# Performance work log

Hardware: AMD Instinct MI355X
Metric: run time of the kernel (lower is better)

The kernel has to match this reference:

```python
import jax, jax.numpy as jnp
import numpy as np

LMBDA = 100.0
GAMMA = 0.5
EPS_EV = 1e-10


def _safe_evals(e):
    return jnp.clip(jnp.nan_to_num(e, nan=EPS_EV, posinf=1e6, neginf=EPS_EV), EPS_EV, None)


def get_mask(evals1, evals2, gamma):
    # evals1, evals2: [B, K]; returns D: [B, K, K] with D[b,i,j] from (evals2[b,i], evals1[b,j])
    e1 = _safe_evals(evals1)
    e2 = _safe_evals(evals2)
    scale = jnp.clip(jnp.maximum(e1.max(axis=1), e2.max(axis=1)), 1e-10, None)[:, None]
    e1 = e1 / scale
    e2 = e2 / scale
    g1 = e1 ** gamma  # [B,K] -> broadcast as column index j
    g2 = e2 ** gamma  # [B,K] -> broadcast as row index i
    d1 = g1 * g1 + 1.0
    d2 = g2 * g2 + 1.0
    M_re = (g2 / d2)[:, :, None] - (g1 / d1)[:, None, :]
    M_im = (1.0 / d2)[:, :, None] - (1.0 / d1)[:, None, :]
    return jnp.nan_to_num(M_re * M_re + M_im * M_im, nan=0.0, posinf=1e6, neginf=0.0)


def setup_inputs() -> dict:
    key = jax.random.key(0)
    k = jax.random.split(key, 6)
    B, N, K, C = 8, 20000, 128, 256
    return {
        "feat_x": jax.random.normal(k[0], (B, N, C), dtype=jnp.float32),
        "feat_y": jax.random.normal(k[1], (B, N, C), dtype=jnp.float32),
        "evals_x": jax.random.uniform(k[2], (B, K), dtype=jnp.float32),
        "evals_y": jax.random.uniform(k[3], (B, K), dtype=jnp.float32),
        "evecs_trans_x": jax.random.normal(k[4], (B, K, N), dtype=jnp.float32),
        "evecs_trans_y": jax.random.normal(k[5], (B, K, N), dtype=jnp.float32),
    }


def reference(feat_x, feat_y, evals_x, evals_y, evecs_trans_x, evecs_trans_y):
    # Spectral projection of features: [B,K,N] @ [B,N,C] -> [B,K,C]
    A = jnp.einsum('bkn,bnc->bkc', evecs_trans_x, feat_x)
    Bm = jnp.einsum('bkn,bnc->bkc', evecs_trans_y, feat_y)
    D = get_mask(evals_x, evals_y, GAMMA)  # [B,K,K]

    A_A_t = jnp.einsum('bic,bjc->bij', A, A)   # [B,K,K]
    B_A_t = jnp.einsum('bic,bjc->bij', Bm, A)  # [B,K,K]

    K = A.shape[1]
    eye = jnp.eye(K, dtype=A.dtype)
    # lhs[b,i] = A_A_t[b] + lmbda * diag(D[b,i]) + 1e-8 * I  -> [B,K,K,K]
    lhs = A_A_t[:, None, :, :] + LMBDA * (D[..., None] * eye) + 1e-8 * eye
    rhs = B_A_t[..., None]  # [B,K,K,1]; rhs[b,i] = B_A_t[b,i,:]
    Cxy = jnp.linalg.solve(lhs, rhs)[..., 0]  # [B,K,K]; row i of Cxy = solution for eigenvalue i
    return Cxy
```

## Files before the change

kernel.cpp:

```cpp
#include <hip/hip_runtime.h>
#include <math.h>

#define B_ 8
#define N_ 20000
#define K_ 128
#define C_ 256

static_assert(N_ % 32 == 0, "N must be multiple of 32");

constexpr float LMBDA = 100.0f;
constexpr float EPS_EV = 1e-10f;

typedef unsigned int u32x4 __attribute__((ext_vector_type(4)));
typedef short short8_t __attribute__((ext_vector_type(8)));
typedef float f32x4 __attribute__((ext_vector_type(4)));

static __device__ inline void split2(float x0, float x1, unsigned& h, unsigned& l) {
  unsigned u0 = __builtin_bit_cast(unsigned, x0);
  unsigned u1 = __builtin_bit_cast(unsigned, x1);
  h = __builtin_amdgcn_perm(u1, u0, 0x07060302u);
  float r0 = x0 - __builtin_bit_cast(float, u0 & 0xFFFF0000u);
  float r1 = x1 - __builtin_bit_cast(float, u1 & 0xFFFF0000u);
  unsigned v0 = __builtin_bit_cast(unsigned, r0);
  unsigned v1 = __builtin_bit_cast(unsigned, r1);
  v0 += 0x7FFFu + ((v0 >> 16) & 1u);
  v1 += 0x7FFFu + ((v1 >> 16) & 1u);
  l = __builtin_amdgcn_perm(v1, v0, 0x07060302u);
}

#define KFENCE()                                              \
  do {                                                        \
    asm volatile("s_waitcnt lgkmcnt(0)" ::: "memory");        \
    __builtin_amdgcn_sched_barrier(0);                        \
    __builtin_amdgcn_s_barrier();                             \
    __builtin_amdgcn_sched_barrier(0);                        \
  } while (0)

__global__ __launch_bounds__(512, 4)
void proj_mfma(const float* __restrict__ feat_x, const float* __restrict__ feat_y,
               const float* __restrict__ evx, const float* __restrict__ evy,
               float* __restrict__ part, int Sa, int chunk) {
  const int bm = blockIdx.z;
  const int b = bm >> 1, mat = bm & 1;
  const float* __restrict__ E = (mat ? evy : evx) + (size_t)b * K_ * N_;
  const float* __restrict__ F = (mat ? feat_y : feat_x) + (size_t)b * N_ * C_;
  const int c0 = blockIdx.x << 7;
  const int s = blockIdx.y;
  const int nb = s * chunk;
  const int ne = min(N_, nb + chunk);
  const int nt = (ne - nb) >> 5;

  __shared__ unsigned short Ah[2][128][40];
  __shared__ unsigned short Al[2][128][40];
  __shared__ unsigned short Bh[2][128][40];
  __shared__ unsigned short Bl[2][128][40];

  const int t = threadIdx.x;
  const int lane = t & 63, wv = t >> 6;
  const int wm = wv & 3;
  const int wcc = wv >> 2;
  const int lr = lane & 15, lg = lane >> 4;

  const int am = t >> 2, ak = (t & 3) << 3;
  const int cl = t & 127, gq = (t >> 7) << 2;
  const int sigw = ((cl >> 3) & 3) << 1;
  const int slotA = ((gq >> 2) ^ sigw) << 2;
  const int slotB = (((gq >> 2) + 4) ^ sigw) << 2;

  f32x4 acc[2][4];
#pragma unroll
  for (int i = 0; i < 2; ++i)
#pragma unroll
    for (int j = 0; j < 4; ++j) acc[i][j] = (f32x4){0.f, 0.f, 0.f, 0.f};

  struct Stage { float4 a0, a1; float b0, b1, b2, b3, b4, b5, b6, b7; };

  auto LOAD = [&](Stage& st, int n0) {
    const float* ep = E + (size_t)am * N_ + n0 + ak;
    st.a0 = *(const float4*)ep;
    st.a1 = *(const float4*)(ep + 4);
    const float* fp = F + (size_t)(n0 + gq) * C_ + c0 + cl;
    st.b0 = fp[0];
    st.b1 = fp[C_];
    st.b2 = fp[2 * C_];
    st.b3 = fp[3 * C_];
    const float* fp2 = fp + (size_t)16 * C_;
    st.b4 = fp2[0];
    st.b5 = fp2[C_];
    st.b6 = fp2[2 * C_];
    st.b7 = fp2[3 * C_];
  };

  auto WRITE = [&](Stage& st, int p) {
    unsigned h01, l01, h23, l23, h45, l45, h67, l67;
    split2(st.a0.x, st.a0.y, h01, l01);
    split2(st.a0.z, st.a0.w, h23, l23);
    split2(st.a1.x, st.a1.y, h45, l45);
    split2(st.a1.z, st.a1.w, h67, l67);
    *(u32x4*)&Ah[p][am][ak] = (u32x4){h01, h23, h45, h67};
    *(u32x4*)&Al[p][am][ak] = (u32x4){l01, l23, l45, l67};
    split2(st.b0, st.b1, h01, l01);
    split2(st.b2, st.b3, h23, l23);
    *(uint2*)&Bh[p][cl][slotA] = (uint2){h01, h23};
    *(uint2*)&Bl[p][cl][slotA] = (uint2){l01, l23};
    split2(st.b4, st.b5, h45, l45);
    split2(st.b6, st.b7, h67, l67);
    *(uint2*)&Bh[p][cl][slotB] = (uint2){h45, h67};
    *(uint2*)&Bl[p][cl][slotB] = (uint2){l45, l67};
  };

  auto COMPUTE = [&](int p) {
    const int k0 = lg << 3;
    short8_t a_h[2], a_l[2];
#pragma unroll
    for (int mt = 0; mt < 2; ++mt) {
      const int m = (wm << 5) + (mt << 4) + lr;
      a_h[mt] = *(const short8_t*)&Ah[p][m][k0];
      a_l[mt] = *(const short8_t*)&Al[p][m][k0];
    }
#pragma unroll
    for (int ct = 0; ct < 4; ++ct) {
      const int c = (wcc << 6) + (ct << 4) + lr;
      const int sig = ((c >> 3) & 3) << 1;
      const int koff = (((lg << 1) ^ sig)) << 2;
      const short8_t b_h = *(const short8_t*)&Bh[p][c][koff];
      const short8_t b_l = *(const short8_t*)&Bl[p][c][koff];
#pragma unroll
      for (int mt = 0; mt < 2; ++mt) {
        acc[mt][ct] = __builtin_amdgcn_mfma_f32_16x16x32_bf16(a_h[mt], b_h, acc[mt][ct], 0, 0, 0);
        acc[mt][ct] = __builtin_amdgcn_mfma_f32_16x16x32_bf16(a_l[mt], b_h, acc[mt][ct], 0, 0, 0);
        acc[mt][ct] = __builtin_amdgcn_mfma_f32_16x16x32_bf16(a_h[mt], b_l, acc[mt][ct], 0, 0, 0);
      }
    }
  };

  Stage sA, sB;
  LOAD(sA, nb);
  if (nt > 1) LOAD(sB, nb + 32);
  WRITE(sA, 0);
  KFENCE();

  for (int it = 0; it < nt; it += 2) {
    if (it + 1 < nt) WRITE(sB, 1);
    if (it + 2 < nt) LOAD(sA, nb + ((it + 2) << 5));
    COMPUTE(0);
    KFENCE();
    if (it + 1 < nt) {
      if (it + 2 < nt) WRITE(sA, 0);
      if (it + 3 < nt) LOAD(sB, nb + ((it + 3) << 5));
      COMPUTE(1);
      KFENCE();
    }
  }

  float* __restrict__ P = part + ((size_t)bm * Sa + s) * (K_ * C_);
#pragma unroll
  for (int mt = 0; mt < 2; ++mt)
#pragma unroll
    for (int ct = 0; ct < 4; ++ct) {
      const int ccol = c0 + (wcc << 6) + (ct << 4) + lr;
#pragma unroll
      for (int r = 0; r < 4; ++r) {
        const int mrow = (wm << 5) + (mt << 4) + (lg << 2) + r;
        P[(size_t)mrow * C_ + ccol] = acc[mt][ct][r];
      }
    }
}

__global__ void reduce_parts(const float* __restrict__ part, float* __restrict__ AB, int Sa) {
  const int idx4 = blockIdx.x * 256 + threadIdx.x;
  if (idx4 >= 16 * K_ * C_ / 4) return;
  const int per = K_ * C_ / 4;
  const int bm = idx4 / per;
  const int rem4 = idx4 - bm * per;
  float4 v = {0.f, 0.f, 0.f, 0.f};
  for (int s = 0; s < Sa; ++s) {
    const float4 p = *(const float4*)&part[((size_t)bm * Sa + s) * (K_ * C_) + rem4 * 4];
    v.x += p.x; v.y += p.y; v.z += p.z; v.w += p.w;
  }
  *(float4*)&AB[(size_t)idx4 * 4] = v;
}

__global__ __launch_bounds__(256)
void gram_kernel(const float* __restrict__ AB, float* __restrict__ Sm, float* __restrict__ Rm) {
  const int b = blockIdx.x, which = blockIdx.y, qz = blockIdx.z;
  const int iq = (qz & 1) << 6, jq = (qz >> 1) << 6;
  const float* __restrict__ L  = AB + ((size_t)(b * 2 + which)) * (K_ * C_);
  const float* __restrict__ Ar = AB + ((size_t)(b * 2)) * (K_ * C_);
  float* __restrict__ out = (which ? Rm : Sm) + (size_t)b * (K_ * K_);
  const int t = threadIdx.x;
  const int ir = iq + ((t >> 4) << 2), jc = jq + ((t & 15) << 2);
  float acc[4][4] = {};
  for (int c0 = 0; c0 < C_; c0 += 4) {
    float4 li[4], rj[4];
#pragma unroll
    for (int i = 0; i < 4; ++i) li[i] = *(const float4*)(L + (size_t)(ir + i) * C_ + c0);
#pragma unroll
    for (int j = 0; j < 4; ++j) rj[j] = *(const float4*)(Ar + (size_t)(jc + j) * C_ + c0);
#pragma unroll
    for (int i = 0; i < 4; ++i)
#pragma unroll
      for (int j = 0; j < 4; ++j)
        acc[i][j] += li[i].x * rj[j].x + li[i].y * rj[j].y +
                     li[i].z * rj[j].z + li[i].w * rj[j].w;
  }
#pragma unroll
  for (int i = 0; i < 4; ++i)
#pragma unroll
    for (int j = 0; j < 4; ++j) {
      float v = acc[i][j];
      if (!which && (ir + i) == (jc + j)) v += 1e-8f;
      out[(size_t)(ir + i) * K_ + (jc + j)] = v;
    }
}

__global__ void mask_prep(const float* __restrict__ evx, const float* __restrict__ evy,
                          float* __restrict__ PQ) {
  const int b = blockIdx.x, t = threadIdx.x;
  float e1 = evx[b * K_ + t];
  float e2 = evy[b * K_ + t];
  if (e1 != e1) e1 = EPS_EV;
  if (e2 != e2) e2 = EPS_EV;
  e1 = fminf(fmaxf(e1, EPS_EV), 1e6f);
  e2 = fminf(fmaxf(e2, EPS_EV), 1e6f);

  __shared__ float wmax[2];
  float v = fmaxf(e1, e2);
#pragma unroll
  for (int d = 1; d < 64; d <<= 1) v = fmaxf(v, __shfl_xor(v, d, 64));
  if ((t & 63) == 0) wmax[t >> 6] = v;
  __syncthreads();
  const float scale = fmaxf(fmaxf(wmax[0], wmax[1]), 1e-10f);

  const float g1 = sqrtf(e1 / scale);
  const float g2 = sqrtf(e2 / scale);
  const float d1 = fmaf(g1, g1, 1.f);
  const float d2 = fmaf(g2, g2, 1.f);
  float* P = PQ + b * 512;
  P[t]       = g1 / d1;
  P[128 + t] = 1.f / d1;
  P[256 + t] = g2 / d2;
  P[384 + t] = 1.f / d2;
}

__global__ __launch_bounds__(512)
void gj_inverse(const float* __restrict__ Sm, float* __restrict__ Sinv) {
  const int b = blockIdx.x, t = threadIdx.x;
  __shared__ float a[K_ * 132];
  __shared__ float Pi[16 * 20];
  __shared__ float Rp[16 * 132];
  __shared__ float Cp[K_ * 20];
  const float* __restrict__ Sb = Sm + (size_t)b * (K_ * K_);
#pragma unroll
  for (int l = 0; l < 8; ++l) {
    int f = t + (l << 9);
    int i = f >> 5, j = (f & 31) << 2;
    *(float4*)&a[i * 132 + j] = *(const float4*)(Sb + i * K_ + j);
  }
  __syncthreads();

  const int j = t & 127, rr = t >> 7;
  const int lane = t & 63;

  for (int p = 0; p < 8; ++p) {
    const int pb = p << 4;

    if (t < 64) {
      const int r = lane & 15, g = lane >> 4;
      float4 v4 = *(const float4*)&a[(pb + r) * 132 + pb + (g << 2)];
      float vv[4] = {v4.x, v4.y, v4.z, v4.w};
#pragma unroll
      for (int k = 0; k < 16; ++k) {
        const int srcrow = (lane & 48) | k;
        float rk[4];
        rk[0] = __shfl(vv[0], srcrow);
        rk[1] = __shfl(vv[1], srcrow);
        rk[2] = __shfl(vv[2], srcrow);
        rk[3] = __shfl(vv[3], srcrow);
        const int kg = (k >> 2) << 4;
        const float pv = __shfl(vv[k & 3], kg | k);
        const float c  = __shfl(vv[k & 3], kg | r);
        const float pr = 1.0f / pv;
        float rs[4];
#pragma unroll
        for (int e = 0; e < 4; ++e) rs[e] = rk[e] * pr;
        if (r == k) {
#pragma unroll
          for (int e = 0; e < 4; ++e) vv[e] = rs[e];
          if (g == (k >> 2)) vv[k & 3] = pr;
        } else {
#pragma unroll
          for (int e = 0; e < 4; ++e) vv[e] = fmaf(-c, rs[e], vv[e]);
          if (g == (k >> 2)) vv[k & 3] = -c * pr;
        }
      }
      Pi[r * 20 + (g << 2) + 0] = vv[0];
      Pi[r * 20 + (g << 2) + 1] = vv[1];
      Pi[r * 20 + (g << 2) + 2] = vv[2];
      Pi[r * 20 + (g << 2) + 3] = vv[3];
    }
    __syncthreads();

    {
      float Ak[16];
#pragma unroll
      for (int k = 0; k < 16; ++k) Ak[k] = a[(pb + k) * 132 + j];
      const unsigned jj = (unsigned)(j - pb);
      const int r0 = rr << 2;
#pragma unroll
      for (int q = 0; q < 4; ++q) {
        const int r = r0 + q;
        float acc = 0.f;
#pragma unroll
        for (int k = 0; k < 16; ++k) acc = fmaf(Pi[r * 20 + k], Ak[k], acc);
        Rp[r * 132 + j] = (jj < 16u) ? Pi[r * 20 + jj] : acc;
      }
      const int i = j;
      const int cb = rr << 2;
      float4 cA = *(const float4*)&a[i * 132 + pb + cb];
      *(float4*)&Cp[i * 20 + cb] = cA;
    }
    __syncthreads();

    {
      float Rk[16];
#pragma unroll
      for (int k = 0; k < 16; ++k) Rk[k] = Rp[k * 132 + j];
      const unsigned jj = (unsigned)(j - pb);
      const int i0 = rr << 5;
#pragma unroll 4
      for (int m = 0; m < 32; ++m) {
        const int i = i0 + m;
        const float4 c0 = *(const float4*)&Cp[i * 20];
        const float4 c1 = *(const float4*)&Cp[i * 20 + 4];
        const float4 c2 = *(const float4*)&Cp[i * 20 + 8];
        const float4 c3 = *(const float4*)&Cp[i * 20 + 12];
        float u0 = c0.x * Rk[0] + c0.y * Rk[1] + c0.z * Rk[2] + c0.w * Rk[3];
        float u1 = c1.x * Rk[4] + c1.y * Rk[5] + c1.z * Rk[6] + c1.w * Rk[7];
        float u2 = c2.x * Rk[8] + c2.y * Rk[9] + c2.z * Rk[10] + c2.w * Rk[11];
        float u3 = c3.x * Rk[12] + c3.y * Rk[13] + c3.z * Rk[14] + c3.w * Rk[15];
        const float upd = (u0 + u1) + (u2 + u3);
        const unsigned ii = (unsigned)(i - pb);
        float newv;
        if (ii < 16u) {
          newv = Rk[ii];
        } else {
          const float base = (jj < 16u) ? 0.f : a[i * 132 + j];
          newv = base - upd;
        }
        a[i * 132 + j] = newv;
      }
    }
    __syncthreads();
  }

  float* __restrict__ O = Sinv + (size_t)b * (K_ * K_);
#pragma unroll
  for (int l = 0; l < 8; ++l) {
    int f = t + (l << 9);
    int i = f >> 5, jq = (f & 31) << 2;
    *(float4*)(O + i * K_ + jq) = *(const float4*)&a[i * 132 + jq];
  }
}

__global__ __launch_bounds__(256)
void solve_iter(const float* __restrict__ Rm, const float* __restrict__ Sinv,
                const float* __restrict__ PQ, const float* __restrict__ Xin,
                float* __restrict__ Xout, const int first) {
  const int bb = blockIdx.x;
  const int b = bb >> 2, rb = (bb & 3) << 5;
  const int t = threadIdx.x;
  __shared__ float Tt[32][34];
  __shared__ float Sv[32][132];
  __shared__ float q1[K_], p1[K_], q2l[32], p2l[32];
  {
    const float* P = PQ + b * 512;
    if (t < K_) { q1[t] = P[t]; p1[t] = P[128 + t]; }
    if (t < 32) { q2l[t] = P[256 + rb + t]; p2l[t] = P[384 + rb + t]; }
  }
  __syncthreads();
  const float* __restrict__ Rb = Rm + (size_t)b * (K_ * K_);
  const float* __restrict__ Xb = Xin + (size_t)b * (K_ * K_);
  const float* __restrict__ Si = Sinv + (size_t)b * (K_ * K_);
  const int ir = (t >> 4) << 1, jc = (t & 15) << 3;
  float acc[2][8] = {};

  for (int k0 = 0; k0 < K_; k0 += 32) {
    {
      const int i = t >> 3;
      const int kk = (t & 7) << 2;
      const int k = k0 + kk;
      const int gi = rb + i;
      float4 tv = *(const float4*)(Rb + (size_t)gi * K_ + k);
      if (!first) {
        const float4 x4 = *(const float4*)(Xb + (size_t)gi * K_ + k);
        const float qi = q2l[i], pi = p2l[i];
        float dq, dp, w;
        dq = qi - q1[k + 0]; dp = pi - p1[k + 0]; w = fmaf(dq, dq, dp * dp);
        tv.x = fmaf(-LMBDA * w, x4.x, tv.x);
        dq = qi - q1[k + 1]; dp = pi - p1[k + 1]; w = fmaf(dq, dq, dp * dp);
        tv.y = fmaf(-LMBDA * w, x4.y, tv.y);
        dq = qi - q1[k + 2]; dp = pi - p1[k + 2]; w = fmaf(dq, dq, dp * dp);
        tv.z = fmaf(-LMBDA * w, x4.z, tv.z);
        dq = qi - q1[k + 3]; dp = pi - p1[k + 3]; w = fmaf(dq, dq, dp * dp);
        tv.w = fmaf(-LMBDA * w, x4.w, tv.w);
      }
      Tt[kk + 0][i] = tv.x; Tt[kk + 1][i] = tv.y;
      Tt[kk + 2][i] = tv.z; Tt[kk + 3][i] = tv.w;
    }
#pragma unroll
    for (int l = 0; l < 4; ++l) {
      int f = t + (l << 8);
      int kk = f >> 5, j4 = (f & 31) << 2;
      *(float4*)&Sv[kk][j4] = *(const float4*)(Si + (size_t)(k0 + kk) * K_ + j4);
    }
    __syncthreads();
#pragma unroll
    for (int kk = 0; kk < 32; ++kk) {
      const float2 a2 = *(const float2*)&Tt[kk][ir];
      const float4 b0 = *(const float4*)&Sv[kk][jc];
      const float4 b1 = *(const float4*)&Sv[kk][jc + 4];
      const float bv[8] = {b0.x, b0.y, b0.z, b0.w, b1.x, b1.y, b1.z, b1.w};
#pragma unroll
      for (int jx = 0; jx < 8; ++jx) {
        acc[0][jx] = fmaf(a2.x, bv[jx], acc[0][jx]);
        acc[1][jx] = fmaf(a2.y, bv[jx], acc[1][jx]);
      }
    }
    __syncthreads();
  }

  float* __restrict__ O = Xout + (size_t)b * (K_ * K_);
#pragma unroll
  for (int i = 0; i < 2; ++i) {
    float4 o0 = {acc[i][0], acc[i][1], acc[i][2], acc[i][3]};
    float4 o1 = {acc[i][4], acc[i][5], acc[i][6], acc[i][7]};
    *(float4*)(O + (size_t)(rb + ir + i) * K_ + jc) = o0;
    *(float4*)(O + (size_t)(rb + ir + i) * K_ + jc + 4) = o1;
  }
}

extern "C" void kernel_launch(void* const* d_in, const int* in_sizes, int n_in,
                              void* d_out, int out_size, void* d_ws, size_t ws_size,
                              hipStream_t stream) {
  (void)in_sizes; (void)n_in; (void)out_size;
  const float* feat_x  = (const float*)d_in[0];
  const float* feat_y  = (const float*)d_in[1];
  const float* evals_x = (const float*)d_in[2];
  const float* evals_y = (const float*)d_in[3];
  const float* evtx    = (const float*)d_in[4];
  const float* evty    = (const float*)d_in[5];
  float* out = (float*)d_out;
  float* ws  = (float*)d_ws;

  const size_t KC16 = (size_t)16 * K_ * C_;
  const size_t KK   = (size_t)K_ * K_;
  const size_t fixed = KC16 + 3 * (KK * B_) + 4096 + 2 * (KK * B_);
  const int T = N_ / 32;

  int S = 16, Sa = 16, chunk = 0;
  for (;;) {
    int steps = (T + S - 1) / S;
    chunk = steps * 32;
    Sa = (T + steps - 1) / steps;
    if (((size_t)Sa * KC16 + fixed) * sizeof(float) <= ws_size || S == 1) break;
    S >>= 1;
  }

  float* part = ws;
  float* AB   = part + (size_t)Sa * KC16;
  float* Sm   = AB + KC16;
  float* Rm   = Sm + KK * B_;
  float* Sinv = Rm + KK * B_;
  float* PQ   = Sinv + KK * B_;
  float* X0   = PQ + 4096;
  float* X1   = X0 + KK * B_;

  mask_prep<<<dim3(8), 128, 0, stream>>>(evals_x, evals_y, PQ);
  proj_mfma<<<dim3(2, Sa, 16), 512, 0, stream>>>(feat_x, feat_y, evtx, evty, part, Sa, chunk);
  reduce_parts<<<dim3(16 * K_ * C_ / 4 / 256), 256, 0, stream>>>(part, AB, Sa);
  gram_kernel<<<dim3(8, 2, 4), 256, 0, stream>>>(AB, Sm, Rm);
  gj_inverse<<<dim3(8), 512, 0, stream>>>(Sm, Sinv);
  solve_iter<<<dim3(32), 256, 0, stream>>>(Rm, Sinv, PQ, X0, X0, 1);
  solve_iter<<<dim3(32), 256, 0, stream>>>(Rm, Sinv, PQ, X0, X1, 0);
  solve_iter<<<dim3(32), 256, 0, stream>>>(Rm, Sinv, PQ, X1, out, 0);
}
```

Baseline: 254.2 us.

## Relayout projection LDS tiles, fuse mask prep into 1024-thread inverse, reorder grid

The projection kernel now writes LDS in MFMA-fragment order in a single flat buffer, so each lane reads its operand with one contiguous vector load and no swizzle arithmetic. Each thread now loads 8 consecutive N rows for both operands. The launch grid is reordered so split-K chunks vary fastest. The mask preparation kernel is merged into the Gauss-Jordan inverse kernel, which now runs 1024 threads per block, removing one launch and spreading the elimination across more threads. The trade-offs are more LDS per inverse block, a possibly different bank-conflict pattern, and a simplified split-count choice.

```diff
diff --git a/kernel.cpp b/kernel.cpp
--- a/kernel.cpp
+++ b/kernel.cpp
@@ -44,16 +44,13 @@
   const int b = bm >> 1, mat = bm & 1;
   const float* __restrict__ E = (mat ? evy : evx) + (size_t)b * K_ * N_;
   const float* __restrict__ F = (mat ? feat_y : feat_x) + (size_t)b * N_ * C_;
-  const int c0 = blockIdx.x << 7;
-  const int s = blockIdx.y;
+  const int c0 = blockIdx.y << 7;
+  const int s = blockIdx.x;
   const int nb = s * chunk;
   const int ne = min(N_, nb + chunk);
   const int nt = (ne - nb) >> 5;
 
-  __shared__ unsigned short Ah[2][128][40];
-  __shared__ unsigned short Al[2][128][40];
-  __shared__ unsigned short Bh[2][128][40];
-  __shared__ unsigned short Bl[2][128][40];
+  __shared__ unsigned int LDSU[16384];
 
   const int t = threadIdx.x;
   const int lane = t & 63, wv = t >> 6;
@@ -61,11 +58,13 @@
   const int wcc = wv >> 2;
   const int lr = lane & 15, lg = lane >> 4;
 
-  const int am = t >> 2, ak = (t & 3) << 3;
-  const int cl = t & 127, gq = (t >> 7) << 2;
-  const int sigw = ((cl >> 3) & 3) << 1;
-  const int slotA = ((gq >> 2) ^ sigw) << 2;
-  const int slotB = (((gq >> 2) + 4) ^ sigw) << 2;
+  const int rA = ((t >> 7) << 5) | (((t >> 6) & 1) << 4) | (t & 15);
+  const int oA = (t >> 4) & 3;
+  const int cB = ((t >> 6) << 4) | (t & 15);
+  const int oB = (t >> 4) & 3;
+
+  const float* __restrict__ eb = E + (size_t)rA * N_ + (oA << 3);
+  const float* __restrict__ fb = F + (size_t)(oB << 3) * C_ + c0 + cB;
 
   f32x4 acc[2][4];
 #pragma unroll
@@ -76,55 +75,52 @@
   struct Stage { float4 a0, a1; float b0, b1, b2, b3, b4, b5, b6, b7; };
 
   auto LOAD = [&](Stage& st, int n0) {
-    const float* ep = E + (size_t)am * N_ + n0 + ak;
+    const float* ep = eb + n0;
     st.a0 = *(const float4*)ep;
     st.a1 = *(const float4*)(ep + 4);
-    const float* fp = F + (size_t)(n0 + gq) * C_ + c0 + cl;
+    const float* fp = fb + (size_t)n0 * C_;
     st.b0 = fp[0];
     st.b1 = fp[C_];
     st.b2 = fp[2 * C_];
     st.b3 = fp[3 * C_];
-    const float* fp2 = fp + (size_t)16 * C_;
-    st.b4 = fp2[0];
-    st.b5 = fp2[C_];
-    st.b6 = fp2[2 * C_];
-    st.b7 = fp2[3 * C_];
+    st.b4 = fp[4 * C_];
+    st.b5 = fp[5 * C_];
+    st.b6 = fp[6 * C_];
+    st.b7 = fp[7 * C_];
   };
 
   auto WRITE = [&](Stage& st, int p) {
-    unsigned h01, l01, h23, l23, h45, l45, h67, l67;
-    split2(st.a0.x, st.a0.y, h01, l01);
-    split2(st.a0.z, st.a0.w, h23, l23);
-    split2(st.a1.x, st.a1.y, h45, l45);
-    split2(st.a1.z, st.a1.w, h67, l67);
-    *(u32x4*)&Ah[p][am][ak] = (u32x4){h01, h23, h45, h67};
-    *(u32x4*)&Al[p][am][ak] = (u32x4){l01, l23, l45, l67};
-    split2(st.b0, st.b1, h01, l01);
-    split2(st.b2, st.b3, h23, l23);
-    *(uint2*)&Bh[p][cl][slotA] = (uint2){h01, h23};
-    *(uint2*)&Bl[p][cl][slotA] = (uint2){l01, l23};
-    split2(st.b4, st.b5, h45, l45);
-    split2(st.b6, st.b7, h67, l67);
-    *(uint2*)&Bh[p][cl][slotB] = (uint2){h45, h67};
-    *(uint2*)&Bl[p][cl][slotB] = (uint2){l45, l67};
+    const int base = (p << 13) + (t << 2);
+    unsigned h0, l0, h1, l1, h2, l2, h3, l3;
+    split2(st.a0.x, st.a0.y, h0, l0);
+    split2(st.a0.z, st.a0.w, h1, l1);
+    split2(st.a1.x, st.a1.y, h2, l2);
+    split2(st.a1.z, st.a1.w, h3, l3);
+    *(u32x4*)&LDSU[base]        = (u32x4){h0, h1, h2, h3};
+    *(u32x4*)&LDSU[base + 2048] = (u32x4){l0, l1, l2, l3};
+    split2(st.b0, st.b1, h0, l0);
+    split2(st.b2, st.b3, h1, l1);
+    split2(st.b4, st.b5, h2, l2);
+    split2(st.b6, st.b7, h3, l3);
+    *(u32x4*)&LDSU[base + 4096] = (u32x4){h0, h1, h2, h3};
+    *(u32x4*)&LDSU[base + 6144] = (u32x4){l0, l1, l2, l3};
   };
 
   auto COMPUTE = [&](int p) {
-    const int k0 = lg << 3;
+    const int pb = p << 13;
     short8_t a_h[2], a_l[2];
 #pragma unroll
     for (int mt = 0; mt < 2; ++mt) {
-      const int m = (wm << 5) + (mt << 4) + lr;
-      a_h[mt] = *(const short8_t*)&Ah[p][m][k0];
-      a_l[mt] = *(const short8_t*)&Al[p][m][k0];
+      const int as = pb + (((wm << 1) + mt) << 8) + (lane << 2);
+      a_h[mt] = *(const short8_t*)&LDSU[as];
+      a_l[mt] = *(const short8_t*)&LDSU[as + 2048];
     }
 #pragma unroll
     for (int ct = 0; ct < 4; ++ct) {
-      const int c = (wcc << 6) + (ct << 4) + lr;
-      const int sig = ((c >> 3) & 3) << 1;
-      const int koff = (((lg << 1) ^ sig)) << 2;
-      const short8_t b_h = *(const short8_t*)&Bh[p][c][koff];
-      const short8_t b_l = *(const short8_t*)&Bl[p][c][koff];
+      const int ctg = (wcc << 2) + ct;
+      const int bs = pb + 4096 + (ctg << 8) + (lane << 2);
+      const short8_t b_h = *(const short8_t*)&LDSU[bs];
+      const short8_t b_l = *(const short8_t*)&LDSU[bs + 2048];
 #pragma unroll
       for (int mt = 0; mt < 2; ++mt) {
         acc[mt][ct] = __builtin_amdgcn_mfma_f32_16x16x32_bf16(a_h[mt], b_h, acc[mt][ct], 0, 0, 0);
@@ -214,51 +210,55 @@
     }
 }
 
-__global__ void mask_prep(const float* __restrict__ evx, const float* __restrict__ evy,
-                          float* __restrict__ PQ) {
-  const int b = blockIdx.x, t = threadIdx.x;
-  float e1 = evx[b * K_ + t];
-  float e2 = evy[b * K_ + t];
-  if (e1 != e1) e1 = EPS_EV;
-  if (e2 != e2) e2 = EPS_EV;
-  e1 = fminf(fmaxf(e1, EPS_EV), 1e6f);
-  e2 = fminf(fmaxf(e2, EPS_EV), 1e6f);
-
-  __shared__ float wmax[2];
-  float v = fmaxf(e1, e2);
-#pragma unroll
-  for (int d = 1; d < 64; d <<= 1) v = fmaxf(v, __shfl_xor(v, d, 64));
-  if ((t & 63) == 0) wmax[t >> 6] = v;
-  __syncthreads();
-  const float scale = fmaxf(fmaxf(wmax[0], wmax[1]), 1e-10f);
-
-  const float g1 = sqrtf(e1 / scale);
-  const float g2 = sqrtf(e2 / scale);
-  const float d1 = fmaf(g1, g1, 1.f);
-  const float d2 = fmaf(g2, g2, 1.f);
-  float* P = PQ + b * 512;
-  P[t]       = g1 / d1;
-  P[128 + t] = 1.f / d1;
-  P[256 + t] = g2 / d2;
-  P[384 + t] = 1.f / d2;
-}
-
-__global__ __launch_bounds__(512)
-void gj_inverse(const float* __restrict__ Sm, float* __restrict__ Sinv) {
+__global__ __launch_bounds__(1024)
+void gjm_fused(const float* __restrict__ Sm, const float* __restrict__ evx,
+               const float* __restrict__ evy, float* __restrict__ Sinv,
+               float* __restrict__ PQ) {
   const int b = blockIdx.x, t = threadIdx.x;
   __shared__ float a[K_ * 132];
-  __shared__ float Pi[16 * 20];
-  __shared__ float Rp[16 * 132];
-  __shared__ float Cp[K_ * 20];
+  __shared__ float Tl[K_ * 132];
+  __shared__ float ev[256];
+  __shared__ float wmax[2];
+
+  if (t < 128) {
+    float e1 = evx[b * K_ + t];
+    float e2 = evy[b * K_ + t];
+    if (e1 != e1) e1 = EPS_EV;
+    if (e2 != e2) e2 = EPS_EV;
+    e1 = fminf(fmaxf(e1, EPS_EV), 1e6f);
+    e2 = fminf(fmaxf(e2, EPS_EV), 1e6f);
+    float v = fmaxf(e1, e2);
+#pragma unroll
+    for (int d = 1; d < 64; d <<= 1) v = fmaxf(v, __shfl_xor(v, d, 64));
+    if ((t & 63) == 0) wmax[t >> 6] = v;
+    ev[t] = e1; ev[128 + t] = e2;
+  }
+  __syncthreads();
+  if (t < 128) {
+    const float scale = fmaxf(fmaxf(wmax[0], wmax[1]), 1e-10f);
+    const float g1 = sqrtf(ev[t] / scale);
+    const float g2 = sqrtf(ev[128 + t] / scale);
+    const float d1 = fmaf(g1, g1, 1.f);
+    const float d2 = fmaf(g2, g2, 1.f);
+    float* P = PQ + b * 512;
+    P[t]       = g1 / d1;
+    P[128 + t] = 1.f / d1;
+    P[256 + t] = g2 / d2;
+    P[384 + t] = 1.f / d2;
+  }
+
   const float* __restrict__ Sb = Sm + (size_t)b * (K_ * K_);
 #pragma unroll
-  for (int l = 0; l < 8; ++l) {
-    int f = t + (l << 9);
+  for (int l = 0; l < 4; ++l) {
+    int f = t + (l << 10);
     int i = f >> 5, j = (f & 31) << 2;
     *(float4*)&a[i * 132 + j] = *(const float4*)(Sb + i * K_ + j);
   }
   __syncthreads();
 
+  float* Pi = &Tl[0];
+  float* Rp = &Tl[512];
+  float* Cp = &Tl[4096];
   const int j = t & 127, rr = t >> 7;
   const int lane = t & 63;
 
@@ -306,19 +306,18 @@
 #pragma unroll
       for (int k = 0; k < 16; ++k) Ak[k] = a[(pb + k) * 132 + j];
       const unsigned jj = (unsigned)(j - pb);
-      const int r0 = rr << 2;
-#pragma unroll
-      for (int q = 0; q < 4; ++q) {
-        const int r = r0 + q;
+#pragma unroll
+      for (int q = 0; q < 2; ++q) {
+        const int r = (rr << 1) + q;
         float acc = 0.f;
 #pragma unroll
         for (int k = 0; k < 16; ++k) acc = fmaf(Pi[r * 20 + k], Ak[k], acc);
         Rp[r * 132 + j] = (jj < 16u) ? Pi[r * 20 + jj] : acc;
       }
       const int i = j;
-      const int cb = rr << 2;
-      float4 cA = *(const float4*)&a[i * 132 + pb + cb];
-      *(float4*)&Cp[i * 20 + cb] = cA;
+      const int cb = rr << 1;
+      float2 cA = *(const float2*)&a[i * 132 + pb + cb];
+      *(float2*)&Cp[i * 20 + cb] = cA;
     }
     __syncthreads();
 
@@ -327,9 +326,9 @@
 #pragma unroll
       for (int k = 0; k < 16; ++k) Rk[k] = Rp[k * 132 + j];
       const unsigned jj = (unsigned)(j - pb);
-      const int i0 = rr << 5;
+      const int i0 = rr << 4;
 #pragma unroll 4
-      for (int m = 0; m < 32; ++m) {
+      for (int m = 0; m < 16; ++m) {
         const int i = i0 + m;
         const float4 c0 = *(const float4*)&Cp[i * 20];
         const float4 c1 = *(const float4*)&Cp[i * 20 + 4];
@@ -356,8 +355,8 @@
 
   float* __restrict__ O = Sinv + (size_t)b * (K_ * K_);
 #pragma unroll
-  for (int l = 0; l < 8; ++l) {
-    int f = t + (l << 9);
+  for (int l = 0; l < 4; ++l) {
+    int f = t + (l << 10);
     int i = f >> 5, jq = (f & 31) << 2;
     *(float4*)(O + i * K_ + jq) = *(const float4*)&a[i * 132 + jq];
   }
@@ -458,14 +457,10 @@
   const size_t fixed = KC16 + 3 * (KK * B_) + 4096 + 2 * (KK * B_);
   const int T = N_ / 32;
 
-  int S = 16, Sa = 16, chunk = 0;
-  for (;;) {
-    int steps = (T + S - 1) / S;
-    chunk = steps * 32;
-    Sa = (T + steps - 1) / steps;
-    if (((size_t)Sa * KC16 + fixed) * sizeof(float) <= ws_size || S == 1) break;
-    S >>= 1;
-  }
+  int Sa = ((16 * KC16 + fixed) * sizeof(float) <= ws_size) ? 16 : 8;
+  int steps = (T + Sa - 1) / Sa;
+  int chunk = steps * 32;
+  Sa = (T + steps - 1) / steps;
 
   float* part = ws;
   float* AB   = part + (size_t)Sa * KC16;
@@ -476,11 +471,10 @@
   float* X0   = PQ + 4096;
   float* X1   = X0 + KK * B_;
 
-  mask_prep<<<dim3(8), 128, 0, stream>>>(evals_x, evals_y, PQ);
-  proj_mfma<<<dim3(2, Sa, 16), 512, 0, stream>>>(feat_x, feat_y, evtx, evty, part, Sa, chunk);
+  proj_mfma<<<dim3(Sa, 2, 16), 512, 0, stream>>>(feat_x, feat_y, evtx, evty, part, Sa, chunk);
   reduce_parts<<<dim3(16 * K_ * C_ / 4 / 256), 256, 0, stream>>>(part, AB, Sa);
   gram_kernel<<<dim3(8, 2, 4), 256, 0, stream>>>(AB, Sm, Rm);
-  gj_inverse<<<dim3(8), 512, 0, stream>>>(Sm, Sinv);
+  gjm_fused<<<dim3(8), 1024, 0, stream>>>(Sm, evals_x, evals_y, Sinv, PQ);
   solve_iter<<<dim3(32), 256, 0, stream>>>(Rm, Sinv, PQ, X0, X0, 1);
   solve_iter<<<dim3(32), 256, 0, stream>>>(Rm, Sinv, PQ, X0, X1, 0);
   solve_iter<<<dim3(32), 256, 0, stream>>>(Rm, Sinv, PQ, X1, out, 0);
```

New measurement: 236.8 us. -6.8%, faster.
